# Kernel optimization log

Measured on AMD Instinct MI355X. Metric: run time of the kernel, lower is better.

Reference implementation:

```python
import jax, jax.numpy as jnp
import numpy as np

N_NODES = 50000
F_IN = 128
F_OUT = 128
N_REL = 8
N_BASIS = 4
N_EDGES = 500000  # per relation


def setup_inputs() -> dict:
    key = jax.random.key(0)
    k1, k2, k3, k4, k5, k6 = jax.random.split(key, 6)
    x = jax.random.normal(k1, (N_NODES, F_IN), dtype=jnp.float32)
    # glorot-style scale for basis weights
    scale = np.sqrt(6.0 / (F_IN + F_OUT)).astype(np.float32)
    W_basis = jax.random.uniform(k2, (N_BASIS, F_IN, F_OUT), dtype=jnp.float32, minval=-scale, maxval=scale)
    cscale = np.sqrt(6.0 / (N_REL + N_BASIS)).astype(np.float32)
    W_comp = jax.random.uniform(k3, (N_REL, N_BASIS), dtype=jnp.float32, minval=-cscale, maxval=cscale)
    edge_vals = jax.random.uniform(k4, (N_REL, N_EDGES), dtype=jnp.float32)
    edge_src = jax.random.randint(k5, (N_REL, N_EDGES), 0, N_NODES, dtype=jnp.int32)
    edge_dst = jax.random.randint(k6, (N_REL, N_EDGES), 0, N_NODES, dtype=jnp.int32)
    return {"x": x, "W_basis": W_basis, "W_comp": W_comp,
            "edge_vals": edge_vals, "edge_src": edge_src, "edge_dst": edge_dst}


def reference(x, W_basis, W_comp, edge_vals, edge_src, edge_dst):
    # Basis mixing: per-relation weight W_r = sum_b comp[r,b] * W_basis[b]
    W_rel = jnp.einsum('rb,bio->rio', W_comp, W_basis)          # [R, Fin, Fout]
    # Dense transform per relation: pre_sup_r = x @ W_r
    pre = jnp.einsum('nf,rfo->rno', x, W_rel)                   # [R, N, Fout]
    n = x.shape[0]
    out = jnp.zeros((n, W_basis.shape[-1]), dtype=x.dtype)
    # SpMM per relation as gather + scatter-add, accumulated (tf.add_n)
    for r in range(W_comp.shape[0]):
        msg = edge_vals[r][:, None] * pre[r, edge_src[r]]       # [E, Fout]
        out = out + jax.ops.segment_sum(msg, edge_dst[r], num_segments=n)
    return jax.nn.relu(out)
```

## Files before the change

kernel.cpp:

```cpp
#include <hip/hip_runtime.h>

#define F 128
#define NB 4
#define NR 8
#define KPB 512
#define BCAP 6144
#define EPB 16384
#define MAXBKT 784
#define CAPW 384

typedef __attribute__((ext_vector_type(8))) short bf16x8;
typedef __attribute__((ext_vector_type(4))) float f32x4;
typedef __attribute__((ext_vector_type(2))) float f32x2;
typedef unsigned long long u64;

__device__ __forceinline__ unsigned f2bf(float f) {
    unsigned u = __float_as_uint(f);
    return (u + 0x7FFFu + ((u >> 16) & 1u)) >> 16;
}
__device__ __forceinline__ unsigned f2bf2(float lo, float hi) {
    return f2bf(lo) | (f2bf(hi) << 16);
}

__global__ void cvt_x_kernel(const float4* __restrict__ x4, uint4* __restrict__ xb, int total8) {
    int i = blockIdx.x * blockDim.x + threadIdx.x;
    if (i >= total8) return;
    float4 a = x4[(size_t)i * 2], b = x4[(size_t)i * 2 + 1];
    xb[i] = make_uint4(f2bf2(a.x, a.y), f2bf2(a.z, a.w), f2bf2(b.x, b.y), f2bf2(b.z, b.w));
}

__global__ void cvt_w_kernel(const float* __restrict__ Wb, unsigned short* __restrict__ Bt) {
    int t = blockIdx.x * blockDim.x + threadIdx.x;
    if (t >= F * NB * F) return;
    int o = t >> 9, bk = t & 511, b = bk >> 7, k = bk & 127;
    Bt[t] = (unsigned short)f2bf(Wb[((size_t)b * F + k) * F + o]);
}

__global__ void init_gcur(int* __restrict__ gcur, int nbkt) {
    int i = blockIdx.x * blockDim.x + threadIdx.x;
    if (i < nbkt) gcur[i] = i * BCAP;
}

__global__ __launch_bounds__(1024) void bucket_scatter(const int* __restrict__ es,
                                                       const float* __restrict__ ev,
                                                       const int* __restrict__ ed,
                                                       int* __restrict__ gcur,
                                                       u64* __restrict__ bbuf,
                                                       int E, int nbkt) {
    __shared__ int lcnt[MAXBKT];
    __shared__ int lbase[MAXBKT];
    const int r = blockIdx.y;
    const int e0 = blockIdx.x * EPB;
    const int e1 = min(e0 + EPB, E);
    const size_t ebase = (size_t)r * E;
    const int t = threadIdx.x;
    const int bbuf_end = nbkt * BCAP - 1;

    for (int i = t; i < nbkt; i += 1024) lcnt[i] = 0;
    __syncthreads();

    int dd[16];
#pragma unroll
    for (int k = 0; k < 4; ++k) {
        int base = e0 + k * 4096 + t * 4;
        if (base + 4 <= e1) {
            int4 d4 = *(const int4*)&ed[ebase + base];
            dd[k * 4 + 0] = d4.x; dd[k * 4 + 1] = d4.y;
            dd[k * 4 + 2] = d4.z; dd[k * 4 + 3] = d4.w;
        } else {
#pragma unroll
            for (int u = 0; u < 4; ++u)
                dd[k * 4 + u] = (base + u < e1) ? ed[ebase + base + u] : -1;
        }
    }
#pragma unroll
    for (int k = 0; k < 16; ++k)
        if (dd[k] >= 0) atomicAdd(&lcnt[(dd[k] * NR + r) >> 9], 1);
    __syncthreads();

    for (int i = t; i < nbkt; i += 1024) {
        int c = lcnt[i];
        lbase[i] = c ? atomicAdd(&gcur[i], c) : 0;
        lcnt[i] = 0;
    }
    __syncthreads();

#pragma unroll
    for (int k = 0; k < 4; ++k) {
        int base = e0 + k * 4096 + t * 4;
        if (base + 4 <= e1) {
            int4 s4 = *(const int4*)&es[ebase + base];
            float4 v4 = *(const float4*)&ev[ebase + base];
            int ss[4] = {s4.x, s4.y, s4.z, s4.w};
            float vv[4] = {v4.x, v4.y, v4.z, v4.w};
#pragma unroll
            for (int u = 0; u < 4; ++u) {
                int key = dd[k * 4 + u] * NR + r;
                int b = key >> 9;
                int rk = atomicAdd(&lcnt[b], 1);
                int pos = min(lbase[b] + rk, bbuf_end);
                bbuf[pos] = (u64)((unsigned)(ss[u] & 0xFFFF) | ((unsigned)(key & 511) << 16))
                          | ((u64)(f2bf(vv[u]) << 16) << 32);
            }
        } else {
            for (int u = 0; u < 4; ++u) {
                if (base + u >= e1 || dd[k * 4 + u] < 0) continue;
                int key = dd[k * 4 + u] * NR + r;
                int b = key >> 9;
                int rk = atomicAdd(&lcnt[b], 1);
                int pos = min(lbase[b] + rk, bbuf_end);
                bbuf[pos] = (u64)((unsigned)(es[ebase + base + u] & 0xFFFF) | ((unsigned)(key & 511) << 16))
                          | ((u64)(f2bf(ev[ebase + base + u]) << 16) << 32);
            }
        }
    }
}

__global__ void bt_kernel(const int* __restrict__ gcur, int* __restrict__ bt, int nbkt) {
    int i = blockIdx.x * blockDim.x + threadIdx.x;
    if (i < nbkt) bt[i] = gcur[i] - i * BCAP;
}

__global__ __launch_bounds__(512) void scan_reduce(const int* __restrict__ cnt,
                                                   int* __restrict__ bsum, int M) {
    int base = blockIdx.x * 4096 + threadIdx.x * 8;
    int s = 0;
    if (base + 8 <= M) {
        int4 a = *(const int4*)&cnt[base];
        int4 c = *(const int4*)&cnt[base + 4];
        s = a.x + a.y + a.z + a.w + c.x + c.y + c.z + c.w;
    } else {
        for (int i = base; i < M; ++i) s += cnt[i];
    }
    for (int off = 1; off < 64; off <<= 1) s += __shfl_xor(s, off);
    __shared__ int wsum[8];
    if ((threadIdx.x & 63) == 0) wsum[threadIdx.x >> 6] = s;
    __syncthreads();
    if (threadIdx.x == 0) {
        int t = 0;
#pragma unroll
        for (int k = 0; k < 8; ++k) t += wsum[k];
        bsum[blockIdx.x] = t;
    }
}

__global__ __launch_bounds__(1024) void scan_bsums(const int* __restrict__ bsum,
                                                   int* __restrict__ bbase, int nb) {
    __shared__ int sums[1024];
    int t = threadIdx.x;
    int v = (t < nb) ? bsum[t] : 0;
    sums[t] = v;
    __syncthreads();
    for (int d = 1; d < 1024; d <<= 1) {
        int u = (t >= d) ? sums[t - d] : 0;
        __syncthreads();
        sums[t] += u;
        __syncthreads();
    }
    if (t < nb) bbase[t] = sums[t] - v;
}

__global__ __launch_bounds__(512) void scan_write(const int* __restrict__ cnt,
                                                  const int* __restrict__ bbase,
                                                  int* __restrict__ offs, int M) {
    int t = threadIdx.x;
    int base = blockIdx.x * 4096 + t * 8;
    int ex[8];
    int s = 0;
    if (base + 8 <= M) {
        int4 a = *(const int4*)&cnt[base];
        int4 c = *(const int4*)&cnt[base + 4];
        int tmp[8] = {a.x, a.y, a.z, a.w, c.x, c.y, c.z, c.w};
#pragma unroll
        for (int k = 0; k < 8; ++k) { ex[k] = s; s += tmp[k]; }
    } else {
        for (int k = 0; k < 8; ++k) ex[k] = 0;
        int s2 = 0;
        for (int i = base, k = 0; i < M; ++i, ++k) { ex[k] = s2; s2 += cnt[i]; }
        s = s2;
    }
    __shared__ int sums[512];
    sums[t] = s;
    __syncthreads();
    for (int d = 1; d < 512; d <<= 1) {
        int u = (t >= d) ? sums[t - d] : 0;
        __syncthreads();
        sums[t] += u;
        __syncthreads();
    }
    int tb = bbase[blockIdx.x] + ((t == 0) ? 0 : sums[t - 1]);
    if (base + 8 <= M) {
        *(int4*)&offs[base] = make_int4(tb + ex[0], tb + ex[1], tb + ex[2], tb + ex[3]);
        *(int4*)&offs[base + 4] = make_int4(tb + ex[4], tb + ex[5], tb + ex[6], tb + ex[7]);
    } else {
        for (int i = base, k = 0; i < M; ++i, ++k) offs[i] = tb + ex[k];
    }
}

__global__ __launch_bounds__(512) void densify(const u64* __restrict__ bbuf,
                                               const int* __restrict__ gcur,
                                               const int* __restrict__ boff,
                                               unsigned* __restrict__ payload,
                                               unsigned* __restrict__ segdesc, int M) {
    __shared__ unsigned slo[BCAP];
    __shared__ unsigned shi[BCAP];
    __shared__ int kcnt[KPB];
    __shared__ int koff[KPB];
    __shared__ int kcur[KPB];
    __shared__ int stmp[KPB];
    const int bk = blockIdx.x;
    const int start = bk * BCAP;
    const int cntE = min(gcur[bk] - start, BCAP);
    const int t = threadIdx.x;
    kcnt[t] = 0;
    kcur[t] = 0;
    __syncthreads();
    for (int i = t; i < cntE; i += 512) {
        u64 e = bbuf[start + i];
        unsigned elo = (unsigned)e;
        slo[i] = elo;
        shi[i] = (unsigned)(e >> 32);
        atomicAdd(&kcnt[(elo >> 16) & 511], 1);
    }
    __syncthreads();
    stmp[t] = kcnt[t];
    __syncthreads();
    for (int d = 1; d < KPB; d <<= 1) {
        int v = (t >= d) ? stmp[t - d] : 0;
        __syncthreads();
        stmp[t] += v;
        __syncthreads();
    }
    koff[t] = stmp[t] - kcnt[t];
    __syncthreads();
    const int gb = boff[bk];
    int key = bk * KPB + t;
    if (key < M)
        segdesc[key] = ((unsigned)(gb + koff[t]) << 8) | (unsigned)min(kcnt[t], 255);
    for (int i = t; i < cntE; i += 512) {
        unsigned elo = slo[i];
        int klo = (elo >> 16) & 511;
        int rk = atomicAdd(&kcur[klo], 1);
        payload[gb + koff[klo] + rk] = (elo & 0xFFFFu) | shi[i];
    }
}

__global__ __launch_bounds__(256) void accum_kernel(const unsigned* __restrict__ xb,
                                                    const unsigned* __restrict__ payload,
                                                    const unsigned* __restrict__ segdesc,
                                                    const float* __restrict__ comp,
                                                    unsigned* __restrict__ mix,
                                                    int c0, int c1) {
    __shared__ float4 scomp[NR];
    __shared__ unsigned plds[4 * CAPW];
    if (threadIdx.x < NR) scomp[threadIdx.x] = ((const float4*)comp)[threadIdx.x];
    __syncthreads();
    int wave = threadIdx.x >> 6, lane = threadIdx.x & 63;
    int d = c0 + blockIdx.x * 4 + wave;
    if (d >= c1) return;

    uint4 sA = *(const uint4*)&segdesc[(size_t)d * 8];
    uint4 sB = *(const uint4*)&segdesc[(size_t)d * 8 + 4];
    unsigned s0 = (unsigned)__builtin_amdgcn_readfirstlane((int)sA.x);
    unsigned s1 = (unsigned)__builtin_amdgcn_readfirstlane((int)sA.y);
    unsigned s2 = (unsigned)__builtin_amdgcn_readfirstlane((int)sA.z);
    unsigned s3 = (unsigned)__builtin_amdgcn_readfirstlane((int)sA.w);
    unsigned s4 = (unsigned)__builtin_amdgcn_readfirstlane((int)sB.x);
    unsigned s5 = (unsigned)__builtin_amdgcn_readfirstlane((int)sB.y);
    unsigned s6 = (unsigned)__builtin_amdgcn_readfirstlane((int)sB.z);
    unsigned s7 = (unsigned)__builtin_amdgcn_readfirstlane((int)sB.w);
    const unsigned start = s0 >> 8;
    const int b0 = (int)((s1 >> 8) - start);
    const int b1 = (int)((s2 >> 8) - start);
    const int b2 = (int)((s3 >> 8) - start);
    const int b3 = (int)((s4 >> 8) - start);
    const int b4 = (int)((s5 >> 8) - start);
    const int b5 = (int)((s6 >> 8) - start);
    const int b6 = (int)((s7 >> 8) - start);
    const int b7 = (int)((s7 >> 8) - start + (s7 & 255u));
    const int total = b7;
    auto bval = [&](int c) {
        return c == 0 ? b0 : c == 1 ? b1 : c == 2 ? b2 : c == 3 ? b3
             : c == 4 ? b4 : c == 5 ? b5 : c == 6 ? b6 : b7;
    };

    const unsigned lbase = wave * CAPW;
    const int stg = min(total, CAPW);
    for (int o = lane; o < stg; o += 64)
        plds[lbase + o] = __builtin_nontemporal_load(&payload[start + o]);

    f32x2 a0 = {0.f, 0.f}, a1 = {0.f, 0.f}, a2 = {0.f, 0.f}, a3 = {0.f, 0.f};
    f32x2 sr = {0.f, 0.f};
    int cur = 0;
    int nb = bval(0);
    auto flush = [&]() {
        float4 cw = scomp[cur];
        a0 += sr * cw.x;
        a1 += sr * cw.y;
        a2 += sr * cw.z;
        a3 += sr * cw.w;
        sr = (f32x2){0.f, 0.f};
        ++cur;
        nb = bval(cur < 7 ? cur : 7);
    };

    int i = 0;
    for (; i + 8 <= total; i += 8) {
        unsigned pw[8];
        if (i + 8 <= CAPW) {
#pragma unroll
            for (int k = 0; k < 8; ++k)
                pw[k] = (unsigned)__builtin_amdgcn_readfirstlane((int)plds[lbase + i + k]);
        } else {
#pragma unroll
            for (int k = 0; k < 8; ++k)
                pw[k] = (unsigned)__builtin_amdgcn_readfirstlane((int)payload[start + i + k]);
        }
        unsigned g[8];
#pragma unroll
        for (int k = 0; k < 8; ++k)
            g[k] = xb[(size_t)(pw[k] & 0xFFFFu) * 64 + lane];
#pragma unroll
        for (int k = 0; k < 8; ++k) {
            while (i + k >= nb && cur < 7) flush();
            float v = __uint_as_float(pw[k] & 0xFFFF0000u);
            f32x2 xv = {__uint_as_float(g[k] << 16), __uint_as_float(g[k] & 0xFFFF0000u)};
            sr += xv * v;
        }
    }
    for (; i < total; ++i) {
        unsigned pw = (unsigned)__builtin_amdgcn_readfirstlane(
            (int)((i < CAPW) ? plds[lbase + i] : payload[start + i]));
        unsigned g = xb[(size_t)(pw & 0xFFFFu) * 64 + lane];
        while (i >= nb && cur < 7) flush();
        float v = __uint_as_float(pw & 0xFFFF0000u);
        f32x2 xv = {__uint_as_float(g << 16), __uint_as_float(g & 0xFFFF0000u)};
        sr += xv * v;
    }
    while (cur < 8) {
        float4 cw = scomp[cur];
        a0 += sr * cw.x;
        a1 += sr * cw.y;
        a2 += sr * cw.z;
        a3 += sr * cw.w;
        sr = (f32x2){0.f, 0.f};
        ++cur;
    }

    unsigned* mrow = mix + (size_t)(d - c0) * 256 + lane;
    mrow[0]   = f2bf2(a0.x, a0.y);
    mrow[64]  = f2bf2(a1.x, a1.y);
    mrow[128] = f2bf2(a2.x, a2.y);
    mrow[192] = f2bf2(a3.x, a3.y);
}

__global__ __launch_bounds__(256) void gemm_mfma(const unsigned short* __restrict__ mix,
                                                 const unsigned short* __restrict__ Bt,
                                                 float* __restrict__ out,
                                                 int rows, int gbase, int N) {
    __shared__ unsigned short As[128 * 64];
    __shared__ unsigned short Bs[128 * 64];
    const int t = threadIdx.x;
    const int row0 = blockIdx.x * 128;
    const int w = t >> 6, lane = t & 63;
    f32x4 acc[2][8] = {};

    for (int kt = 0; kt < 8; ++kt) {
        __syncthreads();
        for (int u = t; u < 1024; u += 256) {
            int r = u >> 3, c = u & 7;
            int k8 = c * 8;
            int ks = k8 ^ ((r & 7) << 3);
            uint4 av = make_uint4(0, 0, 0, 0);
            if (row0 + r < rows) av = *(const uint4*)&mix[(size_t)(row0 + r) * 512 + kt * 64 + k8];
            *(uint4*)&As[r * 64 + ks] = av;
            uint4 bv = *(const uint4*)&Bt[(size_t)r * 512 + kt * 64 + k8];
            *(uint4*)&Bs[r * 64 + ks] = bv;
        }
        __syncthreads();
#pragma unroll
        for (int ks = 0; ks < 2; ++ks) {
            bf16x8 a[2], b[8];
            const int kbase = ks * 32 + (lane >> 4) * 8;
#pragma unroll
            for (int i = 0; i < 2; ++i) {
                int r = w * 32 + i * 16 + (lane & 15);
                int kk = kbase ^ ((r & 7) << 3);
                a[i] = *(bf16x8*)&As[r * 64 + kk];
            }
#pragma unroll
            for (int jj = 0; jj < 8; ++jj) {
                int o = jj * 16 + (lane & 15);
                int kk = kbase ^ ((o & 7) << 3);
                b[jj] = *(bf16x8*)&Bs[o * 64 + kk];
            }
#pragma unroll
            for (int i = 0; i < 2; ++i)
#pragma unroll
                for (int jj = 0; jj < 8; ++jj)
                    acc[i][jj] = __builtin_amdgcn_mfma_f32_16x16x32_bf16(a[i], b[jj], acc[i][jj], 0, 0, 0);
        }
    }

#pragma unroll
    for (int i = 0; i < 2; ++i) {
        int mbase = w * 32 + i * 16 + (lane >> 4) * 4;
#pragma unroll
        for (int q = 0; q < 4; ++q) {
            int m = mbase + q;
            int gr = gbase + row0 + m;
            if (row0 + m < rows && gr < N) {
#pragma unroll
                for (int jj = 0; jj < 8; ++jj) {
                    int n = jj * 16 + (lane & 15);
                    out[(size_t)gr * F + n] = fmaxf(acc[i][jj][q], 0.f);
                }
            }
        }
    }
}

extern "C" void kernel_launch(void* const* d_in, const int* in_sizes, int n_in,
                              void* d_out, int out_size, void* d_ws, size_t ws_size,
                              hipStream_t stream) {
    const float* x  = (const float*)d_in[0];
    const float* Wb = (const float*)d_in[1];
    const float* Wc = (const float*)d_in[2];
    const float* ev = (const float*)d_in[3];
    const int*   es = (const int*)d_in[4];
    const int*   ed = (const int*)d_in[5];
    float* out = (float*)d_out;

    const int N = in_sizes[0] / F;
    const int E = in_sizes[3] / NR;
    const int M = NR * N;
    const int nbkt = (M + KPB - 1) / KPB;
    const int nb2 = (nbkt + 4095) / 4096;

    char* p = (char*)d_ws;
    auto alloc = [&](size_t bytes) -> char* {
        char* q = p;
        p += (bytes + 255) & ~(size_t)255;
        return q;
    };
    u64* bbuf          = (u64*)alloc((size_t)nbkt * BCAP * 8);
    unsigned* payload  = (unsigned*)alloc((size_t)NR * E * 4);
    int* gcur          = (int*)alloc((size_t)nbkt * 4);
    int* bt            = (int*)alloc((size_t)nbkt * 4);
    int* bsum          = (int*)alloc((size_t)(nb2 + 16) * 4);
    int* bbase         = (int*)alloc((size_t)(nb2 + 16) * 4);
    int* boff          = (int*)alloc((size_t)nbkt * 4);
    unsigned* segdesc  = (unsigned*)alloc((size_t)M * 4);
    unsigned short* Bt = (unsigned short*)alloc((size_t)F * NB * F * 2);
    unsigned* xb       = (unsigned*)alloc((size_t)N * F * 2);

    size_t used = (size_t)(p - (char*)d_ws);
    size_t rem = ws_size > used ? ws_size - used : (size_t)(128 * 1024);
    size_t mix_rows = (rem / (512 * 2)) & ~(size_t)127;
    int chunk = (int)(mix_rows < 128 ? 128
                      : (mix_rows > (size_t)N ? (size_t)((N + 127) & ~(size_t)127) : mix_rows));
    unsigned short* mixbuf = (unsigned short*)p;

    cvt_x_kernel<<<(N * F / 8 + 255) / 256, 256, 0, stream>>>((const float4*)x, (uint4*)xb, N * F / 8);
    cvt_w_kernel<<<(F * NB * F + 255) / 256, 256, 0, stream>>>(Wb, Bt);
    init_gcur<<<(nbkt + 255) / 256, 256, 0, stream>>>(gcur, nbkt);

    dim3 bg((E + EPB - 1) / EPB, NR);
    bucket_scatter<<<bg, 1024, 0, stream>>>(es, ev, ed, gcur, bbuf, E, nbkt);

    bt_kernel<<<(nbkt + 255) / 256, 256, 0, stream>>>(gcur, bt, nbkt);
    scan_reduce<<<nb2, 512, 0, stream>>>(bt, bsum, nbkt);
    scan_bsums<<<1, 1024, 0, stream>>>(bsum, bbase, nb2);
    scan_write<<<nb2, 512, 0, stream>>>(bt, bbase, boff, nbkt);

    densify<<<nbkt, 512, 0, stream>>>(bbuf, gcur, boff, payload, segdesc, M);

    for (int c0 = 0; c0 < N; c0 += chunk) {
        int crows = min(chunk, N - c0);
        accum_kernel<<<(crows + 3) / 4, 256, 0, stream>>>(xb, payload, segdesc, Wc,
                                                          (unsigned*)mixbuf, c0, c0 + crows);
        gemm_mfma<<<(crows + 127) / 128, 256, 0, stream>>>(mixbuf, Bt, out, crows, c0, N);
    }
}
```

Before: 225.7 us.

## Split feature gather into four column-quarter passes over a quartered x layout

Stores the bf16 copy of x as four column-quarter planes of 64 bytes per node, and runs the edge accumulation four times, once per quarter. Each wave handles 4 edges at once, 16 lanes per edge, then reduces the partial sums across lane groups with shuffles. The aim is a gathered working set per pass small enough to stay in cache, and more edges in flight per wave. In exchange, the payload and segment descriptors are re-read four times, and there is extra shuffle-reduction work and more kernel launches.

```diff
diff --git a/kernel.cpp b/kernel.cpp
--- a/kernel.cpp
+++ b/kernel.cpp
@@ -22,11 +22,14 @@
     return f2bf(lo) | (f2bf(hi) << 16);
 }
 
-__global__ void cvt_x_kernel(const float4* __restrict__ x4, uint4* __restrict__ xb, int total8) {
-    int i = blockIdx.x * blockDim.x + threadIdx.x;
-    if (i >= total8) return;
-    float4 a = x4[(size_t)i * 2], b = x4[(size_t)i * 2 + 1];
-    xb[i] = make_uint4(f2bf2(a.x, a.y), f2bf2(a.z, a.w), f2bf2(b.x, b.y), f2bf2(b.z, b.w));
+__global__ void cvt_xq_kernel(const float* __restrict__ x, unsigned* __restrict__ xq, int N) {
+    int tid = blockIdx.x * blockDim.x + threadIdx.x;
+    if (tid >= N * 64) return;
+    int n = tid >> 6, p = tid & 63;
+    int q = p >> 4, fl = p & 15;
+    float lo = x[(size_t)n * 128 + p * 2];
+    float hi = x[(size_t)n * 128 + p * 2 + 1];
+    xq[((size_t)q * N + n) * 16 + fl] = f2bf2(lo, hi);
 }
 
 __global__ void cvt_w_kernel(const float* __restrict__ Wb, unsigned short* __restrict__ Bt) {
@@ -245,18 +248,22 @@
     }
 }
 
-__global__ __launch_bounds__(256) void accum_kernel(const unsigned* __restrict__ xb,
-                                                    const unsigned* __restrict__ payload,
-                                                    const unsigned* __restrict__ segdesc,
-                                                    const float* __restrict__ comp,
-                                                    unsigned* __restrict__ mix,
-                                                    int c0, int c1) {
-    __shared__ float4 scomp[NR];
+__global__ __launch_bounds__(256) void accum_q(const unsigned* __restrict__ xq,
+                                               const unsigned* __restrict__ payload,
+                                               const unsigned* __restrict__ segdesc,
+                                               const float* __restrict__ comp,
+                                               unsigned* __restrict__ mix,
+                                               int qoff, int c0, int c1) {
+    __shared__ f32x4 scomp4[NR];
     __shared__ unsigned plds[4 * CAPW];
-    if (threadIdx.x < NR) scomp[threadIdx.x] = ((const float4*)comp)[threadIdx.x];
-    __syncthreads();
-    int wave = threadIdx.x >> 6, lane = threadIdx.x & 63;
-    int d = c0 + blockIdx.x * 4 + wave;
+    if (threadIdx.x < NR) {
+        float4 c = ((const float4*)comp)[threadIdx.x];
+        scomp4[threadIdx.x] = (f32x4){c.x, c.y, c.z, c.w};
+    }
+    __syncthreads();
+    const int wave = threadIdx.x >> 6, lane = threadIdx.x & 63;
+    const int g = lane >> 4, fl = lane & 15;
+    const int d = c0 + blockIdx.x * 4 + wave;
     if (d >= c1) return;
 
     uint4 sA = *(const uint4*)&segdesc[(size_t)d * 8];
@@ -293,65 +300,63 @@
     f32x2 sr = {0.f, 0.f};
     int cur = 0;
     int nb = bval(0);
-    auto flush = [&]() {
-        float4 cw = scomp[cur];
-        a0 += sr * cw.x;
-        a1 += sr * cw.y;
-        a2 += sr * cw.z;
-        a3 += sr * cw.w;
-        sr = (f32x2){0.f, 0.f};
-        ++cur;
-        nb = bval(cur < 7 ? cur : 7);
-    };
-
-    int i = 0;
-    for (; i + 8 <= total; i += 8) {
-        unsigned pw[8];
-        if (i + 8 <= CAPW) {
-#pragma unroll
-            for (int k = 0; k < 8; ++k)
-                pw[k] = (unsigned)__builtin_amdgcn_readfirstlane((int)plds[lbase + i + k]);
-        } else {
-#pragma unroll
-            for (int k = 0; k < 8; ++k)
-                pw[k] = (unsigned)__builtin_amdgcn_readfirstlane((int)payload[start + i + k]);
-        }
-        unsigned g[8];
-#pragma unroll
-        for (int k = 0; k < 8; ++k)
-            g[k] = xb[(size_t)(pw[k] & 0xFFFFu) * 64 + lane];
-#pragma unroll
-        for (int k = 0; k < 8; ++k) {
-            while (i + k >= nb && cur < 7) flush();
+    const int steps = (total + 3) >> 2;
+
+    for (int sb = 0; sb < steps; sb += 4) {
+        unsigned pw[4], gx[4];
+#pragma unroll
+        for (int k = 0; k < 4; ++k) {
+            int idx = (sb + k) * 4 + g;
+            bool valid = idx < total;
+            unsigned p = 0;
+            if (valid) p = (idx < CAPW) ? plds[lbase + idx] : payload[start + idx];
+            pw[k] = p;
+            gx[k] = valid ? xq[(size_t)(p & 0xFFFFu) * 16 + fl] : 0u;
+        }
+#pragma unroll
+        for (int k = 0; k < 4; ++k) {
+            int idx = (sb + k) * 4 + g;
+            while (idx >= nb && cur < 7) {
+                f32x4 cw = scomp4[cur];
+                a0 += sr * cw.x;
+                a1 += sr * cw.y;
+                a2 += sr * cw.z;
+                a3 += sr * cw.w;
+                sr = (f32x2){0.f, 0.f};
+                ++cur;
+                nb = bval(cur < 7 ? cur : 7);
+            }
             float v = __uint_as_float(pw[k] & 0xFFFF0000u);
-            f32x2 xv = {__uint_as_float(g[k] << 16), __uint_as_float(g[k] & 0xFFFF0000u)};
+            f32x2 xv = {__uint_as_float(gx[k] << 16), __uint_as_float(gx[k] & 0xFFFF0000u)};
             sr += xv * v;
         }
     }
-    for (; i < total; ++i) {
-        unsigned pw = (unsigned)__builtin_amdgcn_readfirstlane(
-            (int)((i < CAPW) ? plds[lbase + i] : payload[start + i]));
-        unsigned g = xb[(size_t)(pw & 0xFFFFu) * 64 + lane];
-        while (i >= nb && cur < 7) flush();
-        float v = __uint_as_float(pw & 0xFFFF0000u);
-        f32x2 xv = {__uint_as_float(g << 16), __uint_as_float(g & 0xFFFF0000u)};
-        sr += xv * v;
-    }
-    while (cur < 8) {
-        float4 cw = scomp[cur];
-        a0 += sr * cw.x;
-        a1 += sr * cw.y;
-        a2 += sr * cw.z;
-        a3 += sr * cw.w;
-        sr = (f32x2){0.f, 0.f};
-        ++cur;
-    }
-
-    unsigned* mrow = mix + (size_t)(d - c0) * 256 + lane;
-    mrow[0]   = f2bf2(a0.x, a0.y);
-    mrow[64]  = f2bf2(a1.x, a1.y);
-    mrow[128] = f2bf2(a2.x, a2.y);
-    mrow[192] = f2bf2(a3.x, a3.y);
+#pragma unroll
+    for (int r = 0; r < 8; ++r) {
+        if (cur < 8) {
+            f32x4 cw = scomp4[cur];
+            a0 += sr * cw.x;
+            a1 += sr * cw.y;
+            a2 += sr * cw.z;
+            a3 += sr * cw.w;
+            sr = (f32x2){0.f, 0.f};
+            ++cur;
+        }
+    }
+#pragma unroll
+    for (int off = 16; off <= 32; off <<= 1) {
+        a0.x += __shfl_xor(a0.x, off); a0.y += __shfl_xor(a0.y, off);
+        a1.x += __shfl_xor(a1.x, off); a1.y += __shfl_xor(a1.y, off);
+        a2.x += __shfl_xor(a2.x, off); a2.y += __shfl_xor(a2.y, off);
+        a3.x += __shfl_xor(a3.x, off); a3.y += __shfl_xor(a3.y, off);
+    }
+    if (g == 0) {
+        unsigned* mrow = mix + (size_t)(d - c0) * 256 + qoff + fl;
+        mrow[0]   = f2bf2(a0.x, a0.y);
+        mrow[64]  = f2bf2(a1.x, a1.y);
+        mrow[128] = f2bf2(a2.x, a2.y);
+        mrow[192] = f2bf2(a3.x, a3.y);
+    }
 }
 
 __global__ __launch_bounds__(256) void gemm_mfma(const unsigned short* __restrict__ mix,
@@ -452,7 +457,7 @@
     int* boff          = (int*)alloc((size_t)nbkt * 4);
     unsigned* segdesc  = (unsigned*)alloc((size_t)M * 4);
     unsigned short* Bt = (unsigned short*)alloc((size_t)F * NB * F * 2);
-    unsigned* xb       = (unsigned*)alloc((size_t)N * F * 2);
+    unsigned* xq       = (unsigned*)alloc((size_t)N * F * 2);
 
     size_t used = (size_t)(p - (char*)d_ws);
     size_t rem = ws_size > used ? ws_size - used : (size_t)(128 * 1024);
@@ -461,7 +466,7 @@
                       : (mix_rows > (size_t)N ? (size_t)((N + 127) & ~(size_t)127) : mix_rows));
     unsigned short* mixbuf = (unsigned short*)p;
 
-    cvt_x_kernel<<<(N * F / 8 + 255) / 256, 256, 0, stream>>>((const float4*)x, (uint4*)xb, N * F / 8);
+    cvt_xq_kernel<<<(N * 64 + 255) / 256, 256, 0, stream>>>(x, xq, N);
     cvt_w_kernel<<<(F * NB * F + 255) / 256, 256, 0, stream>>>(Wb, Bt);
     init_gcur<<<(nbkt + 255) / 256, 256, 0, stream>>>(gcur, nbkt);
 
@@ -477,8 +482,10 @@
 
     for (int c0 = 0; c0 < N; c0 += chunk) {
         int crows = min(chunk, N - c0);
-        accum_kernel<<<(crows + 3) / 4, 256, 0, stream>>>(xb, payload, segdesc, Wc,
-                                                          (unsigned*)mixbuf, c0, c0 + crows);
+        for (int q = 0; q < 4; ++q)
+            accum_q<<<(crows + 3) / 4, 256, 0, stream>>>(
+                xq + (size_t)q * N * 16, payload, segdesc, Wc,
+                (unsigned*)mixbuf, q * 16, c0, c0 + crows);
         gemm_mfma<<<(crows + 127) / 128, 256, 0, stream>>>(mixbuf, Bt, out, crows, c0, N);
     }
 }
```

Result: slower. 417.3 us (+84.8%).
